# Performance work log

Measured on AMD Instinct MI355X. Metric: run time of the kernel, lower is better.

The kernel has to match this reference:

```python
import jax, jax.numpy as jnp
import numpy as np

N = 100000    # nodes
E = 800000    # directed edges
EF = 16       # edge features
NF = 1        # node features (forced by the module's MLP-size constraint)
HID = NF * 8  # NNConv out = 8
H1, C1 = 8, 16  # gat1 heads / per-head channels -> 128
NC = 16       # num_classes (gat2: heads=1, out=NC)


def setup_inputs() -> dict:
    key = jax.random.key(0)
    ks = jax.random.split(key, 20)
    s = 0.1
    return {
        "x": jax.random.normal(ks[0], (N, NF), jnp.float32),
        "edge_index": jax.random.randint(ks[1], (2, E), 0, N, jnp.int64),
        "edge_attr": jax.random.normal(ks[2], (E, EF), jnp.float32),
        # edge MLP: Linear(EF,8) -> ReLU -> Linear(8,8)
        "w1": jax.random.normal(ks[3], (EF, HID), jnp.float32) * s,
        "b1": jnp.zeros((HID,), jnp.float32),
        "w2": jax.random.normal(ks[4], (HID, HID), jnp.float32) * s,
        "b2": jnp.zeros((HID,), jnp.float32),
        # NNConv root weight + bias
        "root": jax.random.normal(ks[5], (NF, HID), jnp.float32) * s,
        "nn_bias": jnp.zeros((HID,), jnp.float32),
        # GAT1: in 8 -> 16 ch x 8 heads
        "g1W": jax.random.normal(ks[6], (HID, H1 * C1), jnp.float32) * s,
        "g1as": jax.random.normal(ks[7], (H1, C1), jnp.float32) * s,
        "g1ad": jax.random.normal(ks[8], (H1, C1), jnp.float32) * s,
        "g1b": jnp.zeros((H1 * C1,), jnp.float32),
        # GAT2: in 128 -> NC, 1 head
        "g2W": jax.random.normal(ks[9], (H1 * C1, NC), jnp.float32) * s,
        "g2as": jax.random.normal(ks[10], (1, NC), jnp.float32) * s,
        "g2ad": jax.random.normal(ks[11], (1, NC), jnp.float32) * s,
        "g2b": jnp.zeros((NC,), jnp.float32),
    }


def _gat(h_in, W, a_src, a_dst, bias, src, dst, n, heads, ch):
    # h: [N, heads, ch]
    h = (h_in @ W).reshape(n, heads, ch)
    e_s = jnp.einsum("nhc,hc->nh", h, a_src)   # per-node src logits
    e_d = jnp.einsum("nhc,hc->nh", h, a_dst)
    e = jax.nn.leaky_relu(e_s[src] + e_d[dst], 0.2)      # [E2, heads]
    m = jax.ops.segment_max(e, dst, num_segments=n)      # segment softmax
    e = jnp.exp(e - m[dst])
    z = jax.ops.segment_sum(e, dst, num_segments=n)
    alpha = e / (z[dst] + 1e-16)                          # [E2, heads]
    out = jax.ops.segment_sum(alpha[:, :, None] * h[src], dst, num_segments=n)
    return out.reshape(n, heads * ch) + bias


def reference(x, edge_index, edge_attr, w1, b1, w2, b2, root, nn_bias,
              g1W, g1as, g1ad, g1b, g2W, g2as, g2ad, g2b):
    n = x.shape[0]
    src, dst = edge_index[0], edge_index[1]

    # ---- NNConv (aggr='mean'): per-edge weight from edge MLP ----
    w_e = jax.nn.relu(edge_attr @ w1 + b1) @ w2 + b2      # [E, NF*HID]
    w_e = w_e.reshape(-1, NF, HID)
    msg = jnp.einsum("ei,eio->eo", x[src], w_e)            # [E, HID]
    sums = jax.ops.segment_sum(msg, dst, num_segments=n)
    cnt = jax.ops.segment_sum(jnp.ones((msg.shape[0],), msg.dtype), dst, num_segments=n)
    aggr = sums / jnp.maximum(cnt, 1.0)[:, None]
    h = jax.nn.relu(aggr + x @ root + nn_bias)             # [N, 8]
    # dropout: eval mode -> identity

    # ---- add self-loops (PyG GATConv default) ----
    loops = jnp.arange(n, dtype=src.dtype)
    src2 = jnp.concatenate([src, loops])
    dst2 = jnp.concatenate([dst, loops])

    h = jax.nn.elu(_gat(h, g1W, g1as, g1ad, g1b, src2, dst2, n, H1, C1))  # [N,128]
    out = _gat(h, g2W, g2as, g2ad, g2b, src2, dst2, n, 1, NC)             # [N,16]
    return jax.nn.log_softmax(out, axis=1)
```

## Files before the change

### kernel.cpp

```cpp
#include <hip/hip_runtime.h>
#include <hip/hip_fp16.h>
#include <math.h>

constexpr int NN  = 100000;
constexpr int NE  = 800000;
constexpr int H1 = 8, C1 = 16;
constexpr int D1 = H1 * C1;
constexpr int NC = 16;
constexpr int SCAN_B = 256;
constexpr int SCAN_NB = (NN + SCAN_B - 1) / SCAN_B;

static inline int cdiv(int a, int b) { return (a + b - 1) / b; }

typedef int   v4i __attribute__((ext_vector_type(4)));
typedef float v2f __attribute__((ext_vector_type(2)));

__device__ inline __half2 h2_bits(unsigned u) {
    __half2 r; __builtin_memcpy(&r, &u, 4); return r;
}
__device__ inline __half2 shflx_h2(__half2 v, int off) {
    int iv; __builtin_memcpy(&iv, &v, 4);
    iv = __shfl_xor(iv, off);
    __half2 r; __builtin_memcpy(&r, &iv, 4); return r;
}

__global__ void hist_kernel(const int* __restrict__ dst, int* __restrict__ deg) {
    int e = blockIdx.x * blockDim.x + threadIdx.x;
    if (e < NE) atomicAdd(&deg[dst[e]], 1);
}

__global__ void scan1(const int* __restrict__ deg, int* __restrict__ row,
                      int* __restrict__ partial) {
    __shared__ int s[SCAN_B];
    int tid = threadIdx.x;
    int i = blockIdx.x * SCAN_B + tid;
    int v = (i < NN) ? deg[i] : 0;
    s[tid] = v;
    __syncthreads();
    for (int off = 1; off < SCAN_B; off <<= 1) {
        int t = 0;
        if (tid >= off) t = s[tid - off];
        __syncthreads();
        s[tid] += t;
        __syncthreads();
    }
    if (i < NN) row[i] = s[tid] - v;
    if (tid == SCAN_B - 1) partial[blockIdx.x] = s[tid];
}

__global__ void scan2(int* __restrict__ partial, int nb) {
    __shared__ int s[512];
    int tid = threadIdx.x;
    int v = (tid < nb) ? partial[tid] : 0;
    s[tid] = v;
    __syncthreads();
    for (int off = 1; off < 512; off <<= 1) {
        int t = 0;
        if (tid >= off) t = s[tid - off];
        __syncthreads();
        s[tid] += t;
        __syncthreads();
    }
    if (tid < nb) partial[tid] = s[tid] - v;
}

__global__ void scan3(int* __restrict__ row, const int* __restrict__ partial,
                      int* __restrict__ cursor) {
    int i = blockIdx.x * SCAN_B + threadIdx.x;
    if (i < NN) {
        int r = row[i] + partial[blockIdx.x];
        row[i] = r;
        cursor[i] = r;
    }
}

__global__ void nnconv_scatter(const float* __restrict__ x,
                               const int* __restrict__ src, const int* __restrict__ dst,
                               const float* __restrict__ ea,
                               const float* __restrict__ w1, const float* __restrict__ b1,
                               const float* __restrict__ w2, const float* __restrict__ b2,
                               int* __restrict__ cursor,
                               int* __restrict__ src_s, __half* __restrict__ msg_s) {
    __shared__ float sw1[16 * 8], sw2[8 * 8], sb1[8], sb2[8];
    int t = threadIdx.x;
    if (t < 128) sw1[t] = w1[t];
    else if (t < 192) sw2[t - 128] = w2[t - 128];
    else if (t < 200) sb1[t - 192] = b1[t - 192];
    else if (t < 208) sb2[t - 200] = b2[t - 200];
    __syncthreads();
    int e = blockIdx.x * blockDim.x + t;
    if (e >= NE) return;

    float a[16];
    const float4* ea4 = (const float4*)(ea + (size_t)e * 16);
    float4 v0 = ea4[0], v1 = ea4[1], v2 = ea4[2], v3 = ea4[3];
    a[0]=v0.x; a[1]=v0.y; a[2]=v0.z; a[3]=v0.w;
    a[4]=v1.x; a[5]=v1.y; a[6]=v1.z; a[7]=v1.w;
    a[8]=v2.x; a[9]=v2.y; a[10]=v2.z; a[11]=v2.w;
    a[12]=v3.x; a[13]=v3.y; a[14]=v3.z; a[15]=v3.w;

    float hdn[8];
#pragma unroll
    for (int j = 0; j < 8; j++) {
        float s = sb1[j];
#pragma unroll
        for (int i = 0; i < 16; i++) s = fmaf(a[i], sw1[i * 8 + j], s);
        hdn[j] = fmaxf(s, 0.f);
    }
    int sn = src[e], dn = dst[e];
    float xv = x[sn];
    __align__(16) __half msg[8];
#pragma unroll
    for (int j = 0; j < 8; j++) {
        float s = sb2[j];
#pragma unroll
        for (int i = 0; i < 8; i++) s = fmaf(hdn[i], sw2[i * 8 + j], s);
        msg[j] = __float2half(xv * s);
    }
    int pos = atomicAdd(&cursor[dn], 1);
    v4i mv; __builtin_memcpy(&mv, msg, 16);
    __builtin_nontemporal_store(mv, (v4i*)(msg_s + (size_t)pos * 8));
    src_s[pos] = sn;
}

__global__ void fused_node1(const float* __restrict__ x,
                            const int* __restrict__ row, const int* __restrict__ deg,
                            const __half* __restrict__ msg_s,
                            const float* __restrict__ root, const float* __restrict__ nb,
                            const float* __restrict__ W,
                            const float* __restrict__ as_, const float* __restrict__ ad_,
                            unsigned char* __restrict__ h1f8,
                            float* __restrict__ es, float* __restrict__ ed) {
    int t = blockIdx.x * blockDim.x + threadIdx.x;
    if (t >= NN * 8) return;
    int n = t >> 3, j = t & 7;
    int rs = row[n], d = deg[n];

    float p0 = 0.f, p1 = 0.f, p2 = 0.f, p3 = 0.f;
    float p4 = 0.f, p5 = 0.f, p6 = 0.f, p7 = 0.f;
    for (int k = j; k < d; k += 8) {
        uint4 m = *(const uint4*)(msg_s + (size_t)(rs + k) * 8);
        float2 f0 = __half22float2(h2_bits(m.x));
        float2 f1 = __half22float2(h2_bits(m.y));
        float2 f2 = __half22float2(h2_bits(m.z));
        float2 f3 = __half22float2(h2_bits(m.w));
        p0 += f0.x; p1 += f0.y; p2 += f1.x; p3 += f1.y;
        p4 += f2.x; p5 += f2.y; p6 += f3.x; p7 += f3.y;
    }
    float k0 = (j & 4) ? p4 : p0, s0 = (j & 4) ? p0 : p4;
    float k1 = (j & 4) ? p5 : p1, s1 = (j & 4) ? p1 : p5;
    float k2 = (j & 4) ? p6 : p2, s2 = (j & 4) ? p2 : p6;
    float k3 = (j & 4) ? p7 : p3, s3 = (j & 4) ? p3 : p7;
    k0 += __shfl_xor(s0, 4); k1 += __shfl_xor(s1, 4);
    k2 += __shfl_xor(s2, 4); k3 += __shfl_xor(s3, 4);
    float m0 = (j & 2) ? k2 : k0, n0 = (j & 2) ? k0 : k2;
    float m1 = (j & 2) ? k3 : k1, n1 = (j & 2) ? k1 : k3;
    m0 += __shfl_xor(n0, 2); m1 += __shfl_xor(n1, 2);
    float q  = (j & 1) ? m1 : m0, r = (j & 1) ? m0 : m1;
    float sum = q + __shfl_xor(r, 1);

    float hj = fmaxf(sum / fmaxf((float)d, 1.f) + x[n] * root[j] + nb[j], 0.f);

    float hv[8];
#pragma unroll
    for (int k = 0; k < 8; k++) hv[k] = __shfl(hj, k, 8);

    int hd = j;
    float acc[16];
#pragma unroll
    for (int c = 0; c < 16; c++) acc[c] = 0.f;
#pragma unroll
    for (int k = 0; k < 8; k++) {
        const float* wr = W + k * D1 + hd * 16;
#pragma unroll
        for (int c = 0; c < 16; c++) acc[c] = fmaf(hv[k], wr[c], acc[c]);
    }
    float s = 0.f, dd = 0.f;
#pragma unroll
    for (int c = 0; c < 16; c++) {
        s = fmaf(acc[c], as_[hd * 16 + c], s);
        dd = fmaf(acc[c], ad_[hd * 16 + c], dd);
    }
    v4i pk;
#pragma unroll
    for (int w = 0; w < 4; w++) {
        int wd = __builtin_amdgcn_cvt_pk_fp8_f32(acc[4*w] * 16.f, acc[4*w+1] * 16.f, 0, false);
        wd = __builtin_amdgcn_cvt_pk_fp8_f32(acc[4*w+2] * 16.f, acc[4*w+3] * 16.f, wd, true);
        pk[w] = wd;
    }
    *(v4i*)(h1f8 + (size_t)n * 128 + hd * 16) = pk;
    es[t] = s;
    ed[t] = dd;
}

__global__ __launch_bounds__(256) void gat1_gather(
        const int* __restrict__ row, const int* __restrict__ deg,
        const int* __restrict__ src_s,
        const float* __restrict__ es, const float* __restrict__ ed,
        const unsigned char* __restrict__ h1f8, const float* __restrict__ b,
        const float* __restrict__ W2,
        const float* __restrict__ as2, const float* __restrict__ ad2,
        __half* __restrict__ h2h, float* __restrict__ es2, float* __restrict__ ed2) {
    __shared__ float sW2[2048];
    __shared__ float so[4][4][132];
    int tid = threadIdx.x;
    for (int idx = tid; idx < 2048; idx += 256) sW2[idx] = W2[idx];
    __syncthreads();

    int wv = tid >> 6, lane = tid & 63;
    int g  = lane >> 4;
    int cl = lane & 15;
    int hd = cl >> 1;
    float4 bv0 = *((const float4*)(b + cl * 8));
    float4 bv1 = *((const float4*)(b + cl * 8 + 4));

    int base = (blockIdx.x * 4 + wv) * 4;
    for (int i = 0; i < 4; i++) {
        int node = base + i;
        int rs = row[node], d = deg[node];
        float edn = ed[node * 8 + hd];

        float vs = es[node * 8 + hd] + edn;
        vs = fmaxf(vs, 0.2f * vs);
        float a0 = (g == 0) ? __expf(vs) : 0.f;
        float z = a0;
        uint2 gl = *(const uint2*)(h1f8 + (size_t)node * 128 + cl * 8);
        v2f d0 = __builtin_amdgcn_cvt_pk_f32_fp8(gl.x, false);
        v2f d1 = __builtin_amdgcn_cvt_pk_f32_fp8(gl.x, true);
        v2f d2 = __builtin_amdgcn_cvt_pk_f32_fp8(gl.y, false);
        v2f d3 = __builtin_amdgcn_cvt_pk_f32_fp8(gl.y, true);
        float c0 = a0 * d0[0], c1 = a0 * d0[1], c2 = a0 * d1[0], c3 = a0 * d1[1];
        float c4 = a0 * d2[0], c5 = a0 * d2[1], c6 = a0 * d3[0], c7 = a0 * d3[1];

        for (int k = g; k < d; k += 4) {
            int s = src_s[rs + k];
            float v = es[(unsigned)s * 8u + hd] + edn;
            v = fmaxf(v, 0.2f * v);
            float a = __expf(v);
            uint2 ge = *(const uint2*)(h1f8 + (size_t)s * 128 + cl * 8);
            v2f e0 = __builtin_amdgcn_cvt_pk_f32_fp8(ge.x, false);
            v2f e1 = __builtin_amdgcn_cvt_pk_f32_fp8(ge.x, true);
            v2f e2 = __builtin_amdgcn_cvt_pk_f32_fp8(ge.y, false);
            v2f e3 = __builtin_amdgcn_cvt_pk_f32_fp8(ge.y, true);
            z += a;
            c0 = fmaf(a, e0[0], c0); c1 = fmaf(a, e0[1], c1);
            c2 = fmaf(a, e1[0], c2); c3 = fmaf(a, e1[1], c3);
            c4 = fmaf(a, e2[0], c4); c5 = fmaf(a, e2[1], c5);
            c6 = fmaf(a, e3[0], c6); c7 = fmaf(a, e3[1], c7);
        }
        z += __shfl_xor(z, 16); z += __shfl_xor(z, 32);
        c0 += __shfl_xor(c0, 16); c0 += __shfl_xor(c0, 32);
        c1 += __shfl_xor(c1, 16); c1 += __shfl_xor(c1, 32);
        c2 += __shfl_xor(c2, 16); c2 += __shfl_xor(c2, 32);
        c3 += __shfl_xor(c3, 16); c3 += __shfl_xor(c3, 32);
        c4 += __shfl_xor(c4, 16); c4 += __shfl_xor(c4, 32);
        c5 += __shfl_xor(c5, 16); c5 += __shfl_xor(c5, 32);
        c6 += __shfl_xor(c6, 16); c6 += __shfl_xor(c6, 32);
        c7 += __shfl_xor(c7, 16); c7 += __shfl_xor(c7, 32);

        float rz = 1.f / (16.f * (z + 1e-16f));
        float o0 = fmaf(c0, rz, bv0.x), o1 = fmaf(c1, rz, bv0.y);
        float o2 = fmaf(c2, rz, bv0.z), o3 = fmaf(c3, rz, bv0.w);
        float o4 = fmaf(c4, rz, bv1.x), o5 = fmaf(c5, rz, bv1.y);
        float o6 = fmaf(c6, rz, bv1.z), o7 = fmaf(c7, rz, bv1.w);
        o0 = o0 > 0.f ? o0 : __expf(o0) - 1.f;
        o1 = o1 > 0.f ? o1 : __expf(o1) - 1.f;
        o2 = o2 > 0.f ? o2 : __expf(o2) - 1.f;
        o3 = o3 > 0.f ? o3 : __expf(o3) - 1.f;
        o4 = o4 > 0.f ? o4 : __expf(o4) - 1.f;
        o5 = o5 > 0.f ? o5 : __expf(o5) - 1.f;
        o6 = o6 > 0.f ? o6 : __expf(o6) - 1.f;
        o7 = o7 > 0.f ? o7 : __expf(o7) - 1.f;
        if (g == 0) {
            float4* sp = (float4*)&so[wv][i][cl * 8];
            sp[0] = make_float4(o0, o1, o2, o3);
            sp[1] = make_float4(o4, o5, o6, o7);
        }
    }
    __asm__ __volatile__("s_waitcnt lgkmcnt(0)" ::: "memory");

    int nl = lane >> 4, c = lane & 15;
    float partial = 0.f;
#pragma unroll 4
    for (int k = 0; k < 128; k += 2) {
        float2 sv = *(const float2*)&so[wv][nl][k];
        partial = fmaf(sv.x, sW2[k * 16 + c], partial);
        partial = fmaf(sv.y, sW2[(k + 1) * 16 + c], partial);
    }
    float ta = partial * as2[c], tb = partial * ad2[c];
#pragma unroll
    for (int off = 1; off < 16; off <<= 1) {
        ta += __shfl_xor(ta, off);
        tb += __shfl_xor(tb, off);
    }
    h2h[(size_t)(base + nl) * 16 + c] = __float2half(partial);
    if (c == 0) { es2[base + nl] = ta; ed2[base + nl] = tb; }
}

__global__ __launch_bounds__(256) void gat2_gather(
        const int* __restrict__ row, const int* __restrict__ deg,
        const int* __restrict__ src_s,
        const float* __restrict__ es, const float* __restrict__ ed,
        const __half* __restrict__ h2h, const float* __restrict__ b,
        float* __restrict__ out) {
    int tid = threadIdx.x;
    int wv = tid >> 6, lane = tid & 63;
    int g = lane >> 3, l = lane & 7;
    const unsigned* h2i = (const unsigned*)h2h;
    float2 bv = ((const float2*)b)[l];
    int base = (blockIdx.x * 4 + wv) * 4;
    for (int i = 0; i < 4; i++) {
        int node = base + i;
        int rs = row[node], d = deg[node];
        float edn = ed[node];
        float vs = es[node] + edn;
        vs = fmaxf(vs, 0.2f * vs);
        float a0 = (g == 0) ? __expf(vs) : 0.f;
        float z = a0;
        __half2 acc = __hmul2(__float2half2_rn(a0),
                              h2_bits(h2i[(unsigned)node * 8u + l]));

        for (int k = g; k < d; k += 8) {
            int s = src_s[rs + k];
            float v = es[s] + edn;
            v = fmaxf(v, 0.2f * v);
            float a = __expf(v);
            unsigned hraw = h2i[(unsigned)s * 8u + l];
            z += a;
            acc = __hfma2(__float2half2_rn(a), h2_bits(hraw), acc);
        }
        z += __shfl_xor(z, 8); z += __shfl_xor(z, 16); z += __shfl_xor(z, 32);
        acc = __hadd2(acc, shflx_h2(acc, 8));
        acc = __hadd2(acc, shflx_h2(acc, 16));
        acc = __hadd2(acc, shflx_h2(acc, 32));

        float rz = 1.f / (z + 1e-16f);
        float2 f = __half22float2(acc);
        float o0 = fmaf(f.x, rz, bv.x);
        float o1 = fmaf(f.y, rz, bv.y);
        float mx = fmaxf(o0, o1);
        mx = fmaxf(mx, __shfl_xor(mx, 1));
        mx = fmaxf(mx, __shfl_xor(mx, 2));
        mx = fmaxf(mx, __shfl_xor(mx, 4));
        float ss = __expf(o0 - mx) + __expf(o1 - mx);
        ss += __shfl_xor(ss, 1); ss += __shfl_xor(ss, 2); ss += __shfl_xor(ss, 4);
        float lg = mx + __logf(ss);
        if (g == 0)
            ((float2*)out)[(unsigned)node * 8u + l] = make_float2(o0 - lg, o1 - lg);
    }
}

extern "C" void kernel_launch(void* const* d_in, const int* in_sizes, int n_in,
                              void* d_out, int out_size, void* d_ws, size_t ws_size,
                              hipStream_t stream) {
    const float* x    = (const float*)d_in[0];
    const int*   ei   = (const int*)d_in[1];
    const float* ea   = (const float*)d_in[2];
    const float* w1   = (const float*)d_in[3];
    const float* b1   = (const float*)d_in[4];
    const float* w2   = (const float*)d_in[5];
    const float* b2   = (const float*)d_in[6];
    const float* root = (const float*)d_in[7];
    const float* nb   = (const float*)d_in[8];
    const float* g1W  = (const float*)d_in[9];
    const float* g1as = (const float*)d_in[10];
    const float* g1ad = (const float*)d_in[11];
    const float* g1b  = (const float*)d_in[12];
    const float* g2W  = (const float*)d_in[13];
    const float* g2as = (const float*)d_in[14];
    const float* g2ad = (const float*)d_in[15];
    const float* g2b  = (const float*)d_in[16];
    float* out = (float*)d_out;

    const int* src = ei;
    const int* dst = ei + NE;

    float* ws = (float*)d_ws;
    size_t o = 0;
    __half* msg_s  = (__half*)(ws + o); o += (size_t)NE * 4;
    unsigned char* h1f8 = (unsigned char*)(ws + o); o += (size_t)NN * 32;
    __half* h2h    = (__half*)(ws + o); o += (size_t)NN * NC / 2;
    int*  src_s = (int*)(ws + o); o += NE;
    int*  deg   = (int*)(ws + o); o += NN;
    int*  row   = (int*)(ws + o); o += NN;
    int*  cur   = (int*)(ws + o); o += NN;
    int*  part  = (int*)(ws + o); o += 512;
    float* es1  = ws + o; o += (size_t)NN * H1;
    float* ed1  = ws + o; o += (size_t)NN * H1;
    float* es2  = ws + o; o += NN;
    float* ed2  = ws + o; o += NN;
    (void)ws_size; (void)in_sizes; (void)n_in; (void)out_size;

    const int B = 256;

    hipMemsetAsync(deg, 0, (size_t)NN * sizeof(int), stream);
    hist_kernel<<<cdiv(NE, B), B, 0, stream>>>(dst, deg);
    scan1<<<SCAN_NB, SCAN_B, 0, stream>>>(deg, row, part);
    scan2<<<1, 512, 0, stream>>>(part, SCAN_NB);
    scan3<<<SCAN_NB, SCAN_B, 0, stream>>>(row, part, cur);

    nnconv_scatter<<<cdiv(NE, B), B, 0, stream>>>(x, src, dst, ea, w1, b1, w2, b2,
                                                  cur, src_s, msg_s);
    fused_node1<<<cdiv(NN * 8, B), B, 0, stream>>>(x, row, deg, msg_s, root, nb,
                                                   g1W, g1as, g1ad, h1f8, es1, ed1);
    gat1_gather<<<NN / 16, B, 0, stream>>>(row, deg, src_s, es1, ed1, h1f8,
                                           g1b, g2W, g2as, g2ad, h2h, es2, ed2);
    gat2_gather<<<NN / 16, B, 0, stream>>>(row, deg, src_s, es2, ed2, h2h, g2b, out);
}
```

Baseline: 328.5 us.

## Merge scan into one atomic-offset kernel, use exp2 logits, prefetch sources

Replaces the three-kernel prefix scan with a single kernel. Each block scans locally and claims its base offset with an atomicAdd on a global total, so CSR segments stay contiguous but blocks are no longer in node order. Attention logits are pre-scaled by log2(e) so the gathers can call the hardware exp2 directly. The gat1 gather loop also prefetches the next source index, and 64-bit index arithmetic becomes unsigned 32-bit. The aim is fewer launches and less per-edge instruction and latency cost, at the price of a nondeterministic edge layout.

```diff
diff --git a/kernel.cpp b/kernel.cpp
--- a/kernel.cpp
+++ b/kernel.cpp
@@ -9,6 +9,7 @@
 constexpr int NC = 16;
 constexpr int SCAN_B = 256;
 constexpr int SCAN_NB = (NN + SCAN_B - 1) / SCAN_B;
+constexpr float LOG2E = 1.44269504f;
 
 static inline int cdiv(int a, int b) { return (a + b - 1) / b; }
 
@@ -29,9 +30,10 @@
     if (e < NE) atomicAdd(&deg[dst[e]], 1);
 }
 
-__global__ void scan1(const int* __restrict__ deg, int* __restrict__ row,
-                      int* __restrict__ partial) {
+__global__ void scan_atomic(const int* __restrict__ deg, int* __restrict__ row,
+                            int* __restrict__ cur, int* __restrict__ total) {
     __shared__ int s[SCAN_B];
+    __shared__ int base;
     int tid = threadIdx.x;
     int i = blockIdx.x * SCAN_B + tid;
     int v = (i < NN) ? deg[i] : 0;
@@ -44,33 +46,12 @@
         s[tid] += t;
         __syncthreads();
     }
-    if (i < NN) row[i] = s[tid] - v;
-    if (tid == SCAN_B - 1) partial[blockIdx.x] = s[tid];
-}
-
-__global__ void scan2(int* __restrict__ partial, int nb) {
-    __shared__ int s[512];
-    int tid = threadIdx.x;
-    int v = (tid < nb) ? partial[tid] : 0;
-    s[tid] = v;
+    if (tid == SCAN_B - 1) base = atomicAdd(total, s[tid]);
     __syncthreads();
-    for (int off = 1; off < 512; off <<= 1) {
-        int t = 0;
-        if (tid >= off) t = s[tid - off];
-        __syncthreads();
-        s[tid] += t;
-        __syncthreads();
-    }
-    if (tid < nb) partial[tid] = s[tid] - v;
-}
-
-__global__ void scan3(int* __restrict__ row, const int* __restrict__ partial,
-                      int* __restrict__ cursor) {
-    int i = blockIdx.x * SCAN_B + threadIdx.x;
     if (i < NN) {
-        int r = row[i] + partial[blockIdx.x];
+        int r = base + s[tid] - v;
         row[i] = r;
-        cursor[i] = r;
+        cur[i] = r;
     }
 }
 
@@ -119,7 +100,7 @@
     }
     int pos = atomicAdd(&cursor[dn], 1);
     v4i mv; __builtin_memcpy(&mv, msg, 16);
-    __builtin_nontemporal_store(mv, (v4i*)(msg_s + (size_t)pos * 8));
+    __builtin_nontemporal_store(mv, (v4i*)(msg_s + (unsigned)pos * 8u));
     src_s[pos] = sn;
 }
 
@@ -139,7 +120,7 @@
     float p0 = 0.f, p1 = 0.f, p2 = 0.f, p3 = 0.f;
     float p4 = 0.f, p5 = 0.f, p6 = 0.f, p7 = 0.f;
     for (int k = j; k < d; k += 8) {
-        uint4 m = *(const uint4*)(msg_s + (size_t)(rs + k) * 8);
+        uint4 m = *(const uint4*)(msg_s + (unsigned)(rs + k) * 8u);
         float2 f0 = __half22float2(h2_bits(m.x));
         float2 f1 = __half22float2(h2_bits(m.y));
         float2 f2 = __half22float2(h2_bits(m.z));
@@ -188,9 +169,9 @@
         wd = __builtin_amdgcn_cvt_pk_fp8_f32(acc[4*w+2] * 16.f, acc[4*w+3] * 16.f, wd, true);
         pk[w] = wd;
     }
-    *(v4i*)(h1f8 + (size_t)n * 128 + hd * 16) = pk;
-    es[t] = s;
-    ed[t] = dd;
+    *(v4i*)(h1f8 + (unsigned)n * 128u + hd * 16) = pk;
+    es[t] = s * LOG2E;
+    ed[t] = dd * LOG2E;
 }
 
 __global__ __launch_bounds__(256) void gat1_gather(
@@ -218,13 +199,14 @@
     for (int i = 0; i < 4; i++) {
         int node = base + i;
         int rs = row[node], d = deg[node];
-        float edn = ed[node * 8 + hd];
-
-        float vs = es[node * 8 + hd] + edn;
+        const int* sp = src_s + rs;
+        float edn = ed[(unsigned)node * 8u + hd];
+
+        float vs = es[(unsigned)node * 8u + hd] + edn;
         vs = fmaxf(vs, 0.2f * vs);
-        float a0 = (g == 0) ? __expf(vs) : 0.f;
+        float a0 = (g == 0) ? __builtin_amdgcn_exp2f(vs) : 0.f;
         float z = a0;
-        uint2 gl = *(const uint2*)(h1f8 + (size_t)node * 128 + cl * 8);
+        uint2 gl = *(const uint2*)(h1f8 + (unsigned)node * 128u + cl * 8);
         v2f d0 = __builtin_amdgcn_cvt_pk_f32_fp8(gl.x, false);
         v2f d1 = __builtin_amdgcn_cvt_pk_f32_fp8(gl.x, true);
         v2f d2 = __builtin_amdgcn_cvt_pk_f32_fp8(gl.y, false);
@@ -232,12 +214,15 @@
         float c0 = a0 * d0[0], c1 = a0 * d0[1], c2 = a0 * d1[0], c3 = a0 * d1[1];
         float c4 = a0 * d2[0], c5 = a0 * d2[1], c6 = a0 * d3[0], c7 = a0 * d3[1];
 
-        for (int k = g; k < d; k += 4) {
-            int s = src_s[rs + k];
+        int k = g;
+        int s = (k < d) ? sp[k] : 0;
+        for (; k < d; k += 4) {
+            int kn = k + 4;
+            int sn = sp[min(kn, d - 1)];
             float v = es[(unsigned)s * 8u + hd] + edn;
             v = fmaxf(v, 0.2f * v);
-            float a = __expf(v);
-            uint2 ge = *(const uint2*)(h1f8 + (size_t)s * 128 + cl * 8);
+            float a = __builtin_amdgcn_exp2f(v);
+            uint2 ge = *(const uint2*)(h1f8 + (unsigned)s * 128u + cl * 8);
             v2f e0 = __builtin_amdgcn_cvt_pk_f32_fp8(ge.x, false);
             v2f e1 = __builtin_amdgcn_cvt_pk_f32_fp8(ge.x, true);
             v2f e2 = __builtin_amdgcn_cvt_pk_f32_fp8(ge.y, false);
@@ -247,6 +232,7 @@
             c2 = fmaf(a, e1[0], c2); c3 = fmaf(a, e1[1], c3);
             c4 = fmaf(a, e2[0], c4); c5 = fmaf(a, e2[1], c5);
             c6 = fmaf(a, e3[0], c6); c7 = fmaf(a, e3[1], c7);
+            s = sn;
         }
         z += __shfl_xor(z, 16); z += __shfl_xor(z, 32);
         c0 += __shfl_xor(c0, 16); c0 += __shfl_xor(c0, 32);
@@ -272,9 +258,9 @@
         o6 = o6 > 0.f ? o6 : __expf(o6) - 1.f;
         o7 = o7 > 0.f ? o7 : __expf(o7) - 1.f;
         if (g == 0) {
-            float4* sp = (float4*)&so[wv][i][cl * 8];
-            sp[0] = make_float4(o0, o1, o2, o3);
-            sp[1] = make_float4(o4, o5, o6, o7);
+            float4* sp2 = (float4*)&so[wv][i][cl * 8];
+            sp2[0] = make_float4(o0, o1, o2, o3);
+            sp2[1] = make_float4(o4, o5, o6, o7);
         }
     }
     __asm__ __volatile__("s_waitcnt lgkmcnt(0)" ::: "memory");
@@ -293,8 +279,11 @@
         ta += __shfl_xor(ta, off);
         tb += __shfl_xor(tb, off);
     }
-    h2h[(size_t)(base + nl) * 16 + c] = __float2half(partial);
-    if (c == 0) { es2[base + nl] = ta; ed2[base + nl] = tb; }
+    h2h[(unsigned)(base + nl) * 16u + c] = __float2half(partial);
+    if (c == 0) {
+        es2[base + nl] = ta * LOG2E;
+        ed2[base + nl] = tb * LOG2E;
+    }
 }
 
 __global__ __launch_bounds__(256) void gat2_gather(
@@ -312,19 +301,20 @@
     for (int i = 0; i < 4; i++) {
         int node = base + i;
         int rs = row[node], d = deg[node];
+        const int* sp = src_s + rs;
         float edn = ed[node];
         float vs = es[node] + edn;
         vs = fmaxf(vs, 0.2f * vs);
-        float a0 = (g == 0) ? __expf(vs) : 0.f;
+        float a0 = (g == 0) ? __builtin_amdgcn_exp2f(vs) : 0.f;
         float z = a0;
         __half2 acc = __hmul2(__float2half2_rn(a0),
                               h2_bits(h2i[(unsigned)node * 8u + l]));
 
         for (int k = g; k < d; k += 8) {
-            int s = src_s[rs + k];
+            int s = sp[k];
             float v = es[s] + edn;
             v = fmaxf(v, 0.2f * v);
-            float a = __expf(v);
+            float a = __builtin_amdgcn_exp2f(v);
             unsigned hraw = h2i[(unsigned)s * 8u + l];
             z += a;
             acc = __hfma2(__float2half2_rn(a), h2_bits(hraw), acc);
@@ -382,9 +372,9 @@
     __half* h2h    = (__half*)(ws + o); o += (size_t)NN * NC / 2;
     int*  src_s = (int*)(ws + o); o += NE;
     int*  deg   = (int*)(ws + o); o += NN;
+    int*  total = (int*)(ws + o); o += 4;
     int*  row   = (int*)(ws + o); o += NN;
     int*  cur   = (int*)(ws + o); o += NN;
-    int*  part  = (int*)(ws + o); o += 512;
     float* es1  = ws + o; o += (size_t)NN * H1;
     float* ed1  = ws + o; o += (size_t)NN * H1;
     float* es2  = ws + o; o += NN;
@@ -393,11 +383,9 @@
 
     const int B = 256;
 
-    hipMemsetAsync(deg, 0, (size_t)NN * sizeof(int), stream);
+    hipMemsetAsync(deg, 0, (size_t)(NN + 4) * sizeof(int), stream);
     hist_kernel<<<cdiv(NE, B), B, 0, stream>>>(dst, deg);
-    scan1<<<SCAN_NB, SCAN_B, 0, stream>>>(deg, row, part);
-    scan2<<<1, 512, 0, stream>>>(part, SCAN_NB);
-    scan3<<<SCAN_NB, SCAN_B, 0, stream>>>(row, part, cur);
+    scan_atomic<<<SCAN_NB, SCAN_B, 0, stream>>>(deg, row, cur, total);
 
     nnconv_scatter<<<cdiv(NE, B), B, 0, stream>>>(x, src, dst, ea, w1, b1, w2, b2,
                                                   cur, src_s, msg_s);
```

Result: no change. 331.3 us (+0.9%).
